# Performance work log

Hardware: AMD Instinct MI355X
Metric: run time of the kernel (lower is better)

The kernel has to match this reference:

```python
import jax, jax.numpy as jnp
import numpy as np

D_MODEL = 1024
D_STATE = 16
D_CONV = 4
D_INNER = 2048  # expand * d_model
DT_RANK = 64    # ceil(d_model / 16)
EPS = 1e-6


def setup_inputs() -> dict:
    key = jax.random.key(0)
    ks = jax.random.split(key, 8)
    B, T = 2, 2048
    x = jax.random.normal(ks[0], (B, T, D_MODEL), dtype=jnp.float32)
    in_proj_w = jax.random.normal(ks[1], (2 * D_INNER, D_MODEL), dtype=jnp.float32) * (D_MODEL ** -0.5)
    conv_w = jax.random.normal(ks[2], (D_INNER, 1, D_CONV), dtype=jnp.float32) * 0.3
    conv_b = jnp.zeros((D_INNER,), dtype=jnp.float32)
    x_proj_w = jax.random.normal(ks[3], (DT_RANK + 2 * D_STATE, D_INNER), dtype=jnp.float32) * (D_INNER ** -0.5)
    dt_std = DT_RANK ** -0.5
    dt_proj_w = jax.random.uniform(ks[4], (D_INNER, DT_RANK), minval=-dt_std, maxval=dt_std, dtype=jnp.float32)
    dt = jnp.exp(jax.random.uniform(ks[5], (D_INNER,), dtype=jnp.float32) * (np.log(0.1) - np.log(0.001)) + np.log(0.001))
    dt_proj_b = dt + jnp.log(-jnp.expm1(-dt))
    A_log = jnp.log(jnp.tile(jnp.arange(1, D_STATE + 1, dtype=jnp.float32)[None, :], (D_INNER, 1)))
    D = jnp.ones((D_INNER,), dtype=jnp.float32)
    out_proj_w = jax.random.normal(ks[6], (D_MODEL, D_INNER), dtype=jnp.float32) * (D_INNER ** -0.5)
    norm_w = jnp.ones((D_MODEL,), dtype=jnp.float32)
    return dict(x=x, in_proj_w=in_proj_w, conv_w=conv_w, conv_b=conv_b,
                x_proj_w=x_proj_w, dt_proj_w=dt_proj_w, dt_proj_b=dt_proj_b,
                A_log=A_log, D=D, out_proj_w=out_proj_w, norm_w=norm_w)


def _mamba_fwd(x, in_proj_w, conv_w, conv_b, x_proj_w, dt_proj_w, dt_proj_b,
               A_log, D, out_proj_w, norm_w):
    residual = x
    # RMSNorm (no mean subtraction)
    xn = x / jnp.sqrt(jnp.mean(x * x, axis=-1, keepdims=True) + EPS) * norm_w
    # in_proj -> [B,T,2*d_inner]
    xz = xn @ in_proj_w.T
    x_s, z = xz[..., :D_INNER], xz[..., D_INNER:]
    # depthwise causal conv1d (left pad d_conv-1, keep first T outputs)
    xc = jax.lax.conv_general_dilated(
        x_s.transpose(0, 2, 1), conv_w, window_strides=(1,),
        padding=[(D_CONV - 1, 0)], dimension_numbers=('NCH', 'OIH', 'NCH'),
        feature_group_count=D_INNER)
    x_conv = jax.nn.silu(xc + conv_b[None, :, None]).transpose(0, 2, 1)  # [B,T,d_inner]
    # x_proj -> (dt_raw, B_ssm, C_ssm)
    x_dbc = x_conv @ x_proj_w.T
    dt_raw = x_dbc[..., :DT_RANK]
    B_ssm = x_dbc[..., DT_RANK:DT_RANK + D_STATE]   # [B,T,d_state]
    C_ssm = x_dbc[..., DT_RANK + D_STATE:]          # [B,T,d_state]
    delta = jax.nn.softplus(dt_raw @ dt_proj_w.T + dt_proj_b)  # [B,T,d_inner]
    A = -jnp.exp(A_log)  # [d_inner, d_state]
    # selective scan (ZOH discretisation) with clamped delta
    dc = jnp.clip(delta, -10.0, 1.0)
    du = dc * x_conv
    Bsz = x.shape[0]
    h0 = jnp.zeros((Bsz, D_INNER, D_STATE), dtype=x.dtype)

    def step(h, inp):
        d_t, du_t, b_t, c_t = inp  # [B,di],[B,di],[B,ds],[B,ds]
        dA = jnp.exp(d_t[:, :, None] * A[None])            # [B,di,ds]
        h = dA * h + du_t[:, :, None] * b_t[:, None, :]
        y = jnp.einsum('bis,bs->bi', h, c_t)
        return h, y

    xs = (dc.transpose(1, 0, 2), du.transpose(1, 0, 2),
          B_ssm.transpose(1, 0, 2), C_ssm.transpose(1, 0, 2))
    _, ys = jax.lax.scan(step, h0, xs)           # ys: [T,B,d_inner]
    y = ys.transpose(1, 0, 2) + x_conv * D       # + skip D term
    y = y * jax.nn.silu(z)                       # gate
    return y @ out_proj_w.T + residual


def reference(x, in_proj_w, conv_w, conv_b, x_proj_w, dt_proj_w, dt_proj_b,
              A_log, D, out_proj_w, norm_w):
    return _mamba_fwd(x, in_proj_w, conv_w, conv_b, x_proj_w, dt_proj_w,
                      dt_proj_b, A_log, D, out_proj_w, norm_w)
```

## Files before the change

kernel.cpp:

```cpp
#include <hip/hip_runtime.h>
#include <hip/hip_bf16.h>

typedef float f32x4 __attribute__((ext_vector_type(4)));
typedef __bf16 bf16x8 __attribute__((ext_vector_type(8)));
typedef unsigned short us8 __attribute__((ext_vector_type(8)));
typedef _Float16 f16x8 __attribute__((ext_vector_type(8)));

#define D_MODEL 1024
#define D_INNER 2048
#define D_STATE 16
#define DT_RANK 64
#define NTOK 4096
#define TSEQ 2048
#define NS32 64

__device__ __forceinline__ unsigned short f2bf(float f) {
  unsigned int u = __builtin_bit_cast(unsigned int, f);
  u += 0x7fffu + ((u >> 16) & 1u);
  return (unsigned short)(u >> 16);
}
__device__ __forceinline__ float bf2f(unsigned short u) {
  return __builtin_bit_cast(float, (unsigned int)u << 16);
}

__device__ __forceinline__ void gload_lds16(const unsigned short* g,
                                            unsigned short* l) {
  __builtin_amdgcn_global_load_lds(
      (const __attribute__((address_space(1))) void*)g,
      (__attribute__((address_space(3))) void*)l, 16, 0, 0);
}

__global__ __launch_bounds__(256) void k_prep(
    const float* __restrict__ x, const float* __restrict__ nw,
    unsigned short* __restrict__ xn,
    const float* __restrict__ w_in, const float* __restrict__ w_xp,
    const float* __restrict__ w_dt, const float* __restrict__ w_out,
    unsigned short* __restrict__ o_in, unsigned short* __restrict__ o_xp,
    unsigned short* __restrict__ o_dt, unsigned short* __restrict__ o_out) {
  int bid = blockIdx.x;
  int tid = threadIdx.x;
  if (bid < 4096) {
    const float4 v = *(const float4*)&x[(size_t)bid * 1024 + tid * 4];
    const float4 w = *(const float4*)&nw[tid * 4];
    float ss = v.x * v.x + v.y * v.y + v.z * v.z + v.w * v.w;
#pragma unroll
    for (int o = 32; o >= 1; o >>= 1) ss += __shfl_xor(ss, o);
    __shared__ float red[4];
    if ((tid & 63) == 0) red[tid >> 6] = ss;
    __syncthreads();
    ss = red[0] + red[1] + red[2] + red[3];
    float rs = rsqrtf(ss * (1.0f / 1024.0f) + 1e-6f);
    ushort4 o4;
    o4.x = f2bf(v.x * rs * w.x);
    o4.y = f2bf(v.y * rs * w.y);
    o4.z = f2bf(v.z * rs * w.z);
    o4.w = f2bf(v.w * rs * w.w);
    *(ushort4*)&xn[(size_t)bid * 1024 + tid * 4] = o4;
    return;
  }
  int idx = (bid - 4096) * 256 + tid;
  const float* src;
  unsigned short* dst;
  int rel;
  if (idx < 1048576) { src = w_in; dst = o_in; rel = idx; }
  else if (idx < 1097728) { src = w_xp; dst = o_xp; rel = idx - 1048576; }
  else if (idx < 1114112) {
    ushort4 z = {0, 0, 0, 0};
    *(ushort4*)&o_xp[196608 + (size_t)(idx - 1097728) * 4] = z;
    return;
  }
  else if (idx < 1146880) { src = w_dt; dst = o_dt; rel = idx - 1114112; }
  else { src = w_out; dst = o_out; rel = idx - 1146880; }
  float4 v = ((const float4*)src)[rel];
  ushort4 o;
  o.x = f2bf(v.x); o.y = f2bf(v.y); o.z = f2bf(v.z); o.w = f2bf(v.w);
  ((ushort4*)dst)[rel] = o;
}

template <int BM, int BN, int WAVES_M, int WAVES_N, int EPI, int KSPLIT>
__device__ __forceinline__ void gemm_body(
    const unsigned short* __restrict__ A, const unsigned short* __restrict__ Bw,
    void* __restrict__ Cout, int M, int N, int K,
    const float* __restrict__ epi) {
  constexpr int BK = 64;
  constexpr int TM = BM / (WAVES_M * 16);
  constexpr int TN = BN / (WAVES_N * 16);
  __shared__ __align__(16) unsigned short As[BM * BK];
  __shared__ __align__(16) unsigned short Bs[BN * BK];
  const int tid = threadIdx.x;
  const int wave = tid >> 6, lane = tid & 63;
  const int wm = wave / WAVES_N, wn = wave % WAVES_N;
  const int m0 = blockIdx.x * BM, n0 = blockIdx.y * BN;
  const int lm = lane & 15, q = lane >> 4;
  const int lrow = lane >> 3;
  const int scol = ((lane & 7) ^ lrow) * 8;

  f32x4 acc[TM][TN] = {};

  const int k0 = (KSPLIT > 0) ? blockIdx.z * KSPLIT : 0;
  const int kend = (KSPLIT > 0) ? k0 + KSPLIT : K;

  for (int kb = k0; kb < kend; kb += BK) {
#pragma unroll
    for (int ii = 0; ii < BM / 32; ++ii) {
      int j = ii * 4 + wave;
      gload_lds16(&A[(size_t)(m0 + j * 8 + lrow) * K + kb + scol],
                  &As[j * 512 + lane * 8]);
    }
#pragma unroll
    for (int ii = 0; ii < BN / 32; ++ii) {
      int j = ii * 4 + wave;
      gload_lds16(&Bw[(size_t)(n0 + j * 8 + lrow) * K + kb + scol],
                  &Bs[j * 512 + lane * 8]);
    }
    __syncthreads();
#pragma unroll
    for (int ks = 0; ks < 2; ++ks) {
      const int pos = ((ks * 4 + q) ^ (lane & 7)) * 8;
      bf16x8 af[TM], bfr[TN];
#pragma unroll
      for (int tm = 0; tm < TM; ++tm)
        af[tm] = __builtin_bit_cast(
            bf16x8, *(const us8*)&As[(wm * TM * 16 + tm * 16 + lm) * BK + pos]);
#pragma unroll
      for (int tn = 0; tn < TN; ++tn)
        bfr[tn] = __builtin_bit_cast(
            bf16x8, *(const us8*)&Bs[(wn * TN * 16 + tn * 16 + lm) * BK + pos]);
#pragma unroll
      for (int tm = 0; tm < TM; ++tm)
#pragma unroll
        for (int tn = 0; tn < TN; ++tn)
          acc[tm][tn] = __builtin_amdgcn_mfma_f32_16x16x32_bf16(
              af[tm], bfr[tn], acc[tm][tn], 0, 0, 0);
    }
    __syncthreads();
  }

#pragma unroll
  for (int tm = 0; tm < TM; ++tm)
#pragma unroll
    for (int tn = 0; tn < TN; ++tn)
#pragma unroll
      for (int r = 0; r < 4; ++r) {
        int mg = m0 + wm * TM * 16 + tm * 16 + q * 4 + r;
        int ng = n0 + wn * TN * 16 + tn * 16 + lm;
        float v = acc[tm][tn][r];
        if (EPI == 0) {
          ((_Float16*)Cout)[(size_t)mg * N + ng] = (_Float16)v;
        } else if (EPI == 2) {
          ((float*)Cout)[(size_t)mg * N + ng] = v + epi[(size_t)mg * N + ng];
        } else if (EPI == 5) {
          if (ng < 96)
            ((float*)Cout)[((size_t)blockIdx.z * NTOK + mg) * 96 + ng] = v;
        }
      }
}

__global__ __launch_bounds__(256) void g_inproj(
    const unsigned short* __restrict__ A, const unsigned short* __restrict__ B,
    void* __restrict__ C) {
  gemm_body<128, 128, 2, 2, 0, 0>(A, B, C, NTOK, 4096, 1024, nullptr);
}
__global__ __launch_bounds__(256) void g_outproj(
    const unsigned short* __restrict__ A, const unsigned short* __restrict__ B,
    void* __restrict__ C, const float* __restrict__ epi) {
  gemm_body<64, 128, 2, 2, 2, 0>(A, B, C, NTOK, 1024, 2048, epi);
}

__global__ __launch_bounds__(256) void g_xprojconv(
    const _Float16* __restrict__ xz, const float* __restrict__ cw,
    const float* __restrict__ cbp, const unsigned short* __restrict__ Bw,
    float* __restrict__ Cout, unsigned short* __restrict__ xcb) {
  constexpr int K = 2048;
  __shared__ __align__(16) unsigned short As[64 * 64];
  __shared__ __align__(16) unsigned short Bs[128 * 64];
  const int tid = threadIdx.x;
  const int wave = tid >> 6, lane = tid & 63;
  const int wm = wave >> 1, wn = wave & 1;
  const int m0 = blockIdx.x * 64, n0 = 0;
  const int lm = lane & 15, q = lane >> 4;
  const int lrow = lane >> 3;
  const int scol = ((lane & 7) ^ lrow) * 8;

  f32x4 acc[2][4] = {};
  const int k0 = blockIdx.z * 256;

  for (int kb = k0; kb < k0 + 256; kb += 64) {
#pragma unroll
    for (int ii = 0; ii < 2; ++ii) {
      int j = ii * 4 + wave;
      int r = j * 8 + lrow;
      int m = m0 + r;
      int t = m & (TSEQ - 1);
      int c = kb + scol;
      float4 cb0 = *(const float4*)&cbp[c];
      float4 cb1 = *(const float4*)&cbp[c + 4];
      float a[8] = {cb0.x, cb0.y, cb0.z, cb0.w, cb1.x, cb1.y, cb1.z, cb1.w};
      float w8[8][4];
#pragma unroll
      for (int e = 0; e < 8; ++e) {
        float4 wv = *(const float4*)&cw[(c + e) * 4];
        w8[e][0] = wv.x; w8[e][1] = wv.y; w8[e][2] = wv.z; w8[e][3] = wv.w;
      }
#pragma unroll
      for (int jj = 0; jj < 4; ++jj) {
        bool ok = (t - 3 + jj) >= 0;
        int msrc = ok ? (m - 3 + jj) : m;
        float g = ok ? 1.0f : 0.0f;
        f16x8 xv = *(const f16x8*)&xz[(size_t)msrc * 4096 + c];
#pragma unroll
        for (int e = 0; e < 8; ++e) a[e] += g * w8[e][jj] * (float)xv[e];
      }
      us8 ov;
#pragma unroll
      for (int e = 0; e < 8; ++e) {
        float sg = 1.0f / (1.0f + __expf(-a[e]));
        ov[e] = f2bf(a[e] * sg);
      }
      *(us8*)&As[j * 512 + lane * 8] = ov;
      *(us8*)&xcb[(size_t)m * 2048 + c] = ov;
    }
#pragma unroll
    for (int ii = 0; ii < 4; ++ii) {
      int j = ii * 4 + wave;
      gload_lds16(&Bw[(size_t)(n0 + j * 8 + lrow) * K + kb + scol],
                  &Bs[j * 512 + lane * 8]);
    }
    __syncthreads();
#pragma unroll
    for (int ks = 0; ks < 2; ++ks) {
      const int pos = ((ks * 4 + q) ^ (lane & 7)) * 8;
      bf16x8 af[2], bfr[4];
#pragma unroll
      for (int tm = 0; tm < 2; ++tm)
        af[tm] = __builtin_bit_cast(
            bf16x8, *(const us8*)&As[(wm * 32 + tm * 16 + lm) * 64 + pos]);
#pragma unroll
      for (int tn = 0; tn < 4; ++tn)
        bfr[tn] = __builtin_bit_cast(
            bf16x8, *(const us8*)&Bs[(wn * 64 + tn * 16 + lm) * 64 + pos]);
#pragma unroll
      for (int tm = 0; tm < 2; ++tm)
#pragma unroll
        for (int tn = 0; tn < 4; ++tn)
          acc[tm][tn] = __builtin_amdgcn_mfma_f32_16x16x32_bf16(
              af[tm], bfr[tn], acc[tm][tn], 0, 0, 0);
    }
    __syncthreads();
  }

#pragma unroll
  for (int tm = 0; tm < 2; ++tm)
#pragma unroll
    for (int tn = 0; tn < 4; ++tn)
#pragma unroll
      for (int r = 0; r < 4; ++r) {
        int mg = m0 + wm * 32 + tm * 16 + q * 4 + r;
        int ng = n0 + wn * 64 + tn * 16 + lm;
        if (ng < 96)
          Cout[((size_t)blockIdx.z * NTOK + mg) * 96 + ng] = acc[tm][tn][r];
      }
}

__global__ __launch_bounds__(256) void k_xreduce(
    const float* __restrict__ part, float* __restrict__ xdbc,
    unsigned short* __restrict__ dtb) {
  int quad = blockIdx.x * 256 + threadIdx.x;
  float4 s = ((const float4*)part)[quad];
#pragma unroll
  for (int z = 1; z < 8; ++z) {
    float4 p = ((const float4*)part)[(size_t)z * 98304 + quad];
    s.x += p.x; s.y += p.y; s.z += p.z; s.w += p.w;
  }
  ((float4*)xdbc)[quad] = s;
  int col4 = (quad % 24) * 4;
  if (col4 < 64) {
    int m = quad / 24;
    ushort4 o;
    o.x = f2bf(s.x); o.y = f2bf(s.y); o.z = f2bf(s.z); o.w = f2bf(s.w);
    *(ushort4*)&dtb[(size_t)m * 64 + col4] = o;
  }
}

__global__ __launch_bounds__(256, 4) void k_dtscan(
    const unsigned short* __restrict__ dtb, const unsigned short* __restrict__ wdt,
    const float* __restrict__ dt_b, const unsigned short* __restrict__ xcb,
    const float* __restrict__ xdbc, _Float16* __restrict__ dcb,
    float* __restrict__ hend32, float* __restrict__ sdc32) {
  __shared__ __align__(16) unsigned short lds[18688];
  _Float16* dcs = (_Float16*)lds;
  float* sB = (float*)&lds[8448];
  unsigned short* xcs = &lds[10496];
  const int tid = threadIdx.x;
  const int wave = tid >> 6, lane = tid & 63;
  const int wm = wave >> 1, wn = wave & 1;
  const int m0 = blockIdx.x * 64, n0 = blockIdx.y * 128;
  const int lm = lane & 15, q = lane >> 4;

#pragma unroll
  for (int i = 0; i < 4; ++i) {
    int flat = i * 256 + tid;
    int t = flat >> 4, c8 = (flat & 15) * 8;
    gload_lds16(&xcb[(size_t)(m0 + t) * 2048 + n0 + c8],
                &xcs[(size_t)flat * 8]);
  }
  {
    int t = tid >> 2, c4 = (tid & 3) * 4;
    gload_lds16((const unsigned short*)&xdbc[(size_t)(m0 + t) * 96 + 64 + c4],
                (unsigned short*)&sB[tid * 4]);
  }

  float bias_v[4];
#pragma unroll
  for (int tn = 0; tn < 4; ++tn) bias_v[tn] = dt_b[n0 + wn * 64 + tn * 16 + lm];

  f32x4 acc[2][4] = {};
  const unsigned short* Ab = &dtb[(size_t)(m0 + wm * 32 + lm) * 64];
  const unsigned short* Bb = &wdt[(size_t)(n0 + wn * 64 + lm) * 64];
#pragma unroll
  for (int ks = 0; ks < 2; ++ks) {
    const int pos = ks * 32 + q * 8;
    bf16x8 af[2], bfr[4];
#pragma unroll
    for (int tm = 0; tm < 2; ++tm)
      af[tm] = __builtin_bit_cast(bf16x8, *(const us8*)&Ab[tm * 1024 + pos]);
#pragma unroll
    for (int tn = 0; tn < 4; ++tn)
      bfr[tn] = __builtin_bit_cast(bf16x8, *(const us8*)&Bb[tn * 1024 + pos]);
#pragma unroll
    for (int tm = 0; tm < 2; ++tm)
#pragma unroll
      for (int tn = 0; tn < 4; ++tn)
        acc[tm][tn] = __builtin_amdgcn_mfma_f32_16x16x32_bf16(
            af[tm], bfr[tn], acc[tm][tn], 0, 0, 0);
  }

  float dck[2][4][4];
#pragma unroll
  for (int tm = 0; tm < 2; ++tm)
#pragma unroll
    for (int tn = 0; tn < 4; ++tn)
#pragma unroll
      for (int r = 0; r < 4; ++r) {
        int mgl = wm * 32 + tm * 16 + q * 4 + r;
        int ngl = wn * 64 + tn * 16 + lm;
        float rr = acc[tm][tn][r] + bias_v[tn];
        float dc = fminf(__logf(1.0f + __expf(rr)), 1.0f);
        dck[tm][tn][r] = dc;
        dcs[mgl * 132 + ngl] = (_Float16)dc;
      }
  __syncthreads();

#pragma unroll
  for (int tm = 0; tm < 2; ++tm)
#pragma unroll
    for (int tn = 0; tn < 4; ++tn)
#pragma unroll
      for (int r = 0; r < 4; ++r) {
        int mgl = wm * 32 + tm * 16 + q * 4 + r;
        int ngl = wn * 64 + tn * 16 + lm;
        dcb[(size_t)(m0 + mgl) * 2048 + n0 + ngl] = (_Float16)dck[tm][tn][r];
      }

  int ch2 = tid & 127, sg = tid >> 7;
  int gch = n0 + ch2;
  int gt0 = m0 + sg * 32;
  int b = gt0 >> 11, s32 = (gt0 & 2047) >> 5;
  size_t base = ((size_t)(b * NS32 + s32) * 2048 + gch);
  float h[16];
#pragma unroll
  for (int s = 0; s < 16; ++s) h[s] = 0.f;
  float Sdc = 0.f;
#pragma unroll 4
  for (int tt = 0; tt < 32; ++tt) {
    int t = sg * 32 + tt;
    float dcv = (float)dcs[t * 132 + ch2];
    float xc = bf2f(xcs[t * 128 + ch2]);
    float qq = __expf(-dcv);
    float du = dcv * xc;
    Sdc += dcv;
    float qp[16];
    qp[0] = qq;
#pragma unroll
    for (int i = 1; i < 16; ++i) qp[i] = qp[i >> 1] * qp[i - (i >> 1) - 1];
    float4 b0 = *(const float4*)&sB[t * 16 + 0];
    float4 b1 = *(const float4*)&sB[t * 16 + 4];
    float4 b2 = *(const float4*)&sB[t * 16 + 8];
    float4 b3 = *(const float4*)&sB[t * 16 + 12];
    float Bv[16] = {b0.x, b0.y, b0.z, b0.w, b1.x, b1.y, b1.z, b1.w,
                    b2.x, b2.y, b2.z, b2.w, b3.x, b3.y, b3.z, b3.w};
#pragma unroll
    for (int s = 0; s < 16; ++s) h[s] = qp[s] * h[s] + du * Bv[s];
  }
#pragma unroll
  for (int s4 = 0; s4 < 4; ++s4)
    *(float4*)&hend32[base * 16 + s4 * 4] = make_float4(
        h[s4 * 4], h[s4 * 4 + 1], h[s4 * 4 + 2], h[s4 * 4 + 3]);
  sdc32[base] = Sdc;
}

__global__ __launch_bounds__(256) void k_scan2(
    const float* __restrict__ hend32, const float* __restrict__ sdc32,
    float* __restrict__ hin32) {
  int idx = blockIdx.x * 256 + threadIdx.x;
  int s = idx & 15, ch = (idx >> 4) & 2047, b = idx >> 15;
  float sp1 = (float)(s + 1);
  float H = 0.f;
  for (int j0 = 0; j0 < NS32; j0 += 8) {
    float he[8], S[8];
#pragma unroll
    for (int k = 0; k < 8; ++k) {
      size_t base = ((size_t)(b * NS32 + j0 + k) * 2048 + ch);
      he[k] = hend32[base * 16 + s];
      S[k] = sdc32[base];
    }
#pragma unroll
    for (int k = 0; k < 8; ++k) {
      size_t base = ((size_t)(b * NS32 + j0 + k) * 2048 + ch);
      hin32[base * 16 + s] = H;
      H = __expf(-S[k] * sp1) * H + he[k];
    }
  }
}

__global__ __launch_bounds__(256) void k_scan3(
    const _Float16* __restrict__ dc, const unsigned short* __restrict__ xcb,
    const float* __restrict__ xdbc, const _Float16* __restrict__ xz,
    const float* __restrict__ hin32, const float* __restrict__ Dp,
    unsigned short* __restrict__ ybf) {
  int bid = blockIdx.x;
  int chg = bid & 7, seg = (bid >> 3) & 63, b = bid >> 9;
  int tid = threadIdx.x;
  int ch = chg * 256 + tid;
  int mbase = b * TSEQ + seg * 32;
  int ch0 = chg * 256;

  __shared__ __align__(16) unsigned short l3[26624];
  _Float16* sdc = (_Float16*)l3;
  unsigned short* sxc = l3 + 8192;
  _Float16* sz = (_Float16*)(l3 + 16384);
  float* sBC = (float*)(l3 + 24576);

#pragma unroll
  for (int i = 0; i < 4; ++i) {
    int flat = i * 256 + tid;
    int tt = flat >> 5, c8 = (flat & 31) * 8;
    gload_lds16((const unsigned short*)&dc[(size_t)(mbase + tt) * 2048 + ch0 + c8],
                (unsigned short*)&sdc[(size_t)flat * 8]);
  }
#pragma unroll
  for (int i = 0; i < 4; ++i) {
    int flat = i * 256 + tid;
    int tt = flat >> 5, c8 = (flat & 31) * 8;
    gload_lds16(&xcb[(size_t)(mbase + tt) * 2048 + ch0 + c8],
                &sxc[(size_t)flat * 8]);
  }
#pragma unroll
  for (int i = 0; i < 4; ++i) {
    int flat = i * 256 + tid;
    int tt = flat >> 5, c8 = (flat & 31) * 8;
    gload_lds16((const unsigned short*)&xz[(size_t)(mbase + tt) * 4096 + 2048 + ch0 + c8],
                (unsigned short*)&sz[(size_t)flat * 8]);
  }
  {
    int t = tid >> 3, c4 = (tid & 7) * 4;
    gload_lds16((const unsigned short*)&xdbc[(size_t)(mbase + t) * 96 + 64 + c4],
                (unsigned short*)&sBC[t * 32 + c4]);
  }

  size_t base = ((size_t)(b * NS32 + seg) * 2048 + ch);
  float h[16];
#pragma unroll
  for (int s4 = 0; s4 < 4; ++s4) {
    float4 hv = *(const float4*)&hin32[base * 16 + s4 * 4];
    h[s4 * 4] = hv.x; h[s4 * 4 + 1] = hv.y;
    h[s4 * 4 + 2] = hv.z; h[s4 * 4 + 3] = hv.w;
  }
  float Dv = Dp[ch];
  __syncthreads();

#pragma unroll 2
  for (int tt = 0; tt < 32; ++tt) {
    float dcv = (float)sdc[tt * 256 + tid];
    float xc = bf2f(sxc[tt * 256 + tid]);
    float z = (float)sz[tt * 256 + tid];
    float qv = __expf(-dcv);
    float du = dcv * xc;
    float qp[16];
    qp[0] = qv;
#pragma unroll
    for (int i = 1; i < 16; ++i) qp[i] = qp[i >> 1] * qp[i - (i >> 1) - 1];
    float4 b0 = *(const float4*)&sBC[tt * 32 + 0];
    float4 b1 = *(const float4*)&sBC[tt * 32 + 4];
    float4 b2 = *(const float4*)&sBC[tt * 32 + 8];
    float4 b3 = *(const float4*)&sBC[tt * 32 + 12];
    float4 c0 = *(const float4*)&sBC[tt * 32 + 16];
    float4 c1 = *(const float4*)&sBC[tt * 32 + 20];
    float4 c2 = *(const float4*)&sBC[tt * 32 + 24];
    float4 c3 = *(const float4*)&sBC[tt * 32 + 28];
    float Bv[16] = {b0.x, b0.y, b0.z, b0.w, b1.x, b1.y, b1.z, b1.w,
                    b2.x, b2.y, b2.z, b2.w, b3.x, b3.y, b3.z, b3.w};
    float Cv[16] = {c0.x, c0.y, c0.z, c0.w, c1.x, c1.y, c1.z, c1.w,
                    c2.x, c2.y, c2.z, c2.w, c3.x, c3.y, c3.z, c3.w};
    float y = 0.f;
#pragma unroll
    for (int s = 0; s < 16; ++s) {
      h[s] = qp[s] * h[s] + du * Bv[s];
      y += h[s] * Cv[s];
    }
    float yv = y + xc * Dv;
    float yf = yv * z / (1.0f + __expf(-z));
    ybf[(size_t)(mbase + tt) * 2048 + ch] = f2bf(yf);
  }
}

extern "C" void kernel_launch(void* const* d_in, const int* in_sizes, int n_in,
                              void* d_out, int out_size, void* d_ws, size_t ws_size,
                              hipStream_t stream) {
  (void)in_sizes; (void)n_in; (void)out_size; (void)ws_size;
  const float* x      = (const float*)d_in[0];
  const float* w_in   = (const float*)d_in[1];
  const float* conv_w = (const float*)d_in[2];
  const float* conv_b = (const float*)d_in[3];
  const float* w_xp   = (const float*)d_in[4];
  const float* w_dt   = (const float*)d_in[5];
  const float* dt_b   = (const float*)d_in[6];
  const float* Dp     = (const float*)d_in[8];
  const float* w_out  = (const float*)d_in[9];
  const float* nw     = (const float*)d_in[10];
  float* out = (float*)d_out;

  char* ws = (char*)d_ws;
  size_t off = 0;
  auto carve = [&](size_t bytes) {
    char* p = ws + off;
    off = (off + bytes + 255) & ~(size_t)255;
    return p;
  };
  unsigned short* xn_bf   = (unsigned short*)carve(8388608);
  unsigned short* w_in_bf = (unsigned short*)carve(8388608);
  unsigned short* w_xp_bf = (unsigned short*)carve(524288);
  unsigned short* w_dt_bf = (unsigned short*)carve(262144);
  unsigned short* w_out_bf= (unsigned short*)carve(4194304);
  _Float16* xz            = (_Float16*)carve(33554432);
  unsigned short* xcb     = (unsigned short*)carve(16777216);
  float* xdbc             = (float*)carve(1572864);
  unsigned short* dtb     = (unsigned short*)carve(524288);
  _Float16* dcb           = (_Float16*)carve(16777216);
  unsigned short* ybf     = (unsigned short*)carve(16777216);
  float* sdc32            = (float*)carve(1048576);
  float* hin32            = (float*)carve(16777216);
  float* xpart            = (float*)carve(12582912);
  float* hend32 = (float*)xn_bf;

  k_prep<<<10624, 256, 0, stream>>>(x, nw, xn_bf, w_in, w_xp, w_dt, w_out,
                                    w_in_bf, w_xp_bf, w_dt_bf, w_out_bf);

  g_inproj<<<dim3(32, 32), 256, 0, stream>>>(xn_bf, w_in_bf, xz);

  g_xprojconv<<<dim3(64, 1, 8), 256, 0, stream>>>(xz, conv_w, conv_b,
                                                  w_xp_bf, xpart, xcb);
  k_xreduce<<<384, 256, 0, stream>>>(xpart, xdbc, dtb);

  k_dtscan<<<dim3(64, 16), 256, 0, stream>>>(dtb, w_dt_bf, dt_b, xcb, xdbc,
                                             dcb, hend32, sdc32);

  k_scan2<<<256, 256, 0, stream>>>(hend32, sdc32, hin32);
  k_scan3<<<1024, 256, 0, stream>>>(dcb, xcb, xdbc, xz, hin32, Dp, ybf);

  g_outproj<<<dim3(64, 8), 256, 0, stream>>>(ybf, w_out_bf, out, x);
}
```

Before: 271.7 us.

## Recompute delta in scan3 instead of storing dcb from dtscan

Drops the fp16 delta buffer that k_dtscan wrote and k_scan3 read back. k_scan3 now recomputes delta for its 32-token by 256-channel tile with a small MFMA over dt_rank, then applies the softplus and clamp. It also streams z from global memory through a 4-deep register prefetch instead of staging it in LDS, which shrinks shared memory and adds an occupancy hint. The cost is that the small dt projection GEMM is now computed twice, and z is read with strided per-thread global loads.

```diff
diff --git a/kernel.cpp b/kernel.cpp
--- a/kernel.cpp
+++ b/kernel.cpp
@@ -285,7 +285,7 @@
 __global__ __launch_bounds__(256, 4) void k_dtscan(
     const unsigned short* __restrict__ dtb, const unsigned short* __restrict__ wdt,
     const float* __restrict__ dt_b, const unsigned short* __restrict__ xcb,
-    const float* __restrict__ xdbc, _Float16* __restrict__ dcb,
+    const float* __restrict__ xdbc,
     float* __restrict__ hend32, float* __restrict__ sdc32) {
   __shared__ __align__(16) unsigned short lds[18688];
   _Float16* dcs = (_Float16*)lds;
@@ -335,7 +335,6 @@
             af[tm], bfr[tn], acc[tm][tn], 0, 0, 0);
   }
 
-  float dck[2][4][4];
 #pragma unroll
   for (int tm = 0; tm < 2; ++tm)
 #pragma unroll
@@ -346,21 +345,9 @@
         int ngl = wn * 64 + tn * 16 + lm;
         float rr = acc[tm][tn][r] + bias_v[tn];
         float dc = fminf(__logf(1.0f + __expf(rr)), 1.0f);
-        dck[tm][tn][r] = dc;
         dcs[mgl * 132 + ngl] = (_Float16)dc;
       }
   __syncthreads();
-
-#pragma unroll
-  for (int tm = 0; tm < 2; ++tm)
-#pragma unroll
-    for (int tn = 0; tn < 4; ++tn)
-#pragma unroll
-      for (int r = 0; r < 4; ++r) {
-        int mgl = wm * 32 + tm * 16 + q * 4 + r;
-        int ngl = wn * 64 + tn * 16 + lm;
-        dcb[(size_t)(m0 + mgl) * 2048 + n0 + ngl] = (_Float16)dck[tm][tn][r];
-      }
 
   int ch2 = tid & 127, sg = tid >> 7;
   int gch = n0 + ch2;
@@ -423,8 +410,9 @@
   }
 }
 
-__global__ __launch_bounds__(256) void k_scan3(
-    const _Float16* __restrict__ dc, const unsigned short* __restrict__ xcb,
+__global__ __launch_bounds__(256, 4) void k_scan3(
+    const unsigned short* __restrict__ dtb, const unsigned short* __restrict__ wdt,
+    const float* __restrict__ dt_b, const unsigned short* __restrict__ xcb,
     const float* __restrict__ xdbc, const _Float16* __restrict__ xz,
     const float* __restrict__ hin32, const float* __restrict__ Dp,
     unsigned short* __restrict__ ybf) {
@@ -435,19 +423,11 @@
   int mbase = b * TSEQ + seg * 32;
   int ch0 = chg * 256;
 
-  __shared__ __align__(16) unsigned short l3[26624];
+  __shared__ __align__(16) unsigned short l3[18432];
   _Float16* sdc = (_Float16*)l3;
   unsigned short* sxc = l3 + 8192;
-  _Float16* sz = (_Float16*)(l3 + 16384);
-  float* sBC = (float*)(l3 + 24576);
-
-#pragma unroll
-  for (int i = 0; i < 4; ++i) {
-    int flat = i * 256 + tid;
-    int tt = flat >> 5, c8 = (flat & 31) * 8;
-    gload_lds16((const unsigned short*)&dc[(size_t)(mbase + tt) * 2048 + ch0 + c8],
-                (unsigned short*)&sdc[(size_t)flat * 8]);
-  }
+  float* sBC = (float*)(l3 + 16384);
+
 #pragma unroll
   for (int i = 0; i < 4; ++i) {
     int flat = i * 256 + tid;
@@ -455,19 +435,51 @@
     gload_lds16(&xcb[(size_t)(mbase + tt) * 2048 + ch0 + c8],
                 &sxc[(size_t)flat * 8]);
   }
-#pragma unroll
-  for (int i = 0; i < 4; ++i) {
-    int flat = i * 256 + tid;
-    int tt = flat >> 5, c8 = (flat & 31) * 8;
-    gload_lds16((const unsigned short*)&xz[(size_t)(mbase + tt) * 4096 + 2048 + ch0 + c8],
-                (unsigned short*)&sz[(size_t)flat * 8]);
-  }
   {
     int t = tid >> 3, c4 = (tid & 7) * 4;
     gload_lds16((const unsigned short*)&xdbc[(size_t)(mbase + t) * 96 + 64 + c4],
                 (unsigned short*)&sBC[t * 32 + c4]);
   }
 
+  const int wave = tid >> 6, lane = tid & 63;
+  const int lm = lane & 15, q = lane >> 4;
+  float bias_v[4];
+#pragma unroll
+  for (int tn = 0; tn < 4; ++tn)
+    bias_v[tn] = dt_b[ch0 + wave * 64 + tn * 16 + lm];
+  f32x4 acc[2][4] = {};
+  const unsigned short* Ab = &dtb[(size_t)(mbase + lm) * 64];
+  const unsigned short* Bb = &wdt[(size_t)(ch0 + wave * 64 + lm) * 64];
+#pragma unroll
+  for (int ks = 0; ks < 2; ++ks) {
+    const int pos = ks * 32 + q * 8;
+    bf16x8 af[2], bfr[4];
+#pragma unroll
+    for (int tm = 0; tm < 2; ++tm)
+      af[tm] = __builtin_bit_cast(bf16x8, *(const us8*)&Ab[tm * 1024 + pos]);
+#pragma unroll
+    for (int tn = 0; tn < 4; ++tn)
+      bfr[tn] = __builtin_bit_cast(bf16x8, *(const us8*)&Bb[tn * 1024 + pos]);
+#pragma unroll
+    for (int tm = 0; tm < 2; ++tm)
+#pragma unroll
+      for (int tn = 0; tn < 4; ++tn)
+        acc[tm][tn] = __builtin_amdgcn_mfma_f32_16x16x32_bf16(
+            af[tm], bfr[tn], acc[tm][tn], 0, 0, 0);
+  }
+#pragma unroll
+  for (int tm = 0; tm < 2; ++tm)
+#pragma unroll
+    for (int tn = 0; tn < 4; ++tn)
+#pragma unroll
+      for (int r = 0; r < 4; ++r) {
+        int t = tm * 16 + q * 4 + r;
+        int c = wave * 64 + tn * 16 + lm;
+        float rr = acc[tm][tn][r] + bias_v[tn];
+        float dc = fminf(__logf(1.0f + __expf(rr)), 1.0f);
+        sdc[t * 256 + c] = (_Float16)dc;
+      }
+
   size_t base = ((size_t)(b * NS32 + seg) * 2048 + ch);
   float h[16];
 #pragma unroll
@@ -477,13 +489,19 @@
     h[s4 * 4 + 2] = hv.z; h[s4 * 4 + 3] = hv.w;
   }
   float Dv = Dp[ch];
+  float zbuf[4];
+#pragma unroll
+  for (int p = 0; p < 4; ++p)
+    zbuf[p] = (float)xz[(size_t)(mbase + p) * 4096 + 2048 + ch];
   __syncthreads();
 
-#pragma unroll 2
+#pragma unroll 4
   for (int tt = 0; tt < 32; ++tt) {
     float dcv = (float)sdc[tt * 256 + tid];
     float xc = bf2f(sxc[tt * 256 + tid]);
-    float z = (float)sz[tt * 256 + tid];
+    float z = zbuf[tt & 3];
+    int tpf = (tt + 4 < 32) ? tt + 4 : 31;
+    zbuf[tt & 3] = (float)xz[(size_t)(mbase + tpf) * 4096 + 2048 + ch];
     float qv = __expf(-dcv);
     float du = dcv * xc;
     float qp[16];
@@ -546,7 +564,6 @@
   unsigned short* xcb     = (unsigned short*)carve(16777216);
   float* xdbc             = (float*)carve(1572864);
   unsigned short* dtb     = (unsigned short*)carve(524288);
-  _Float16* dcb           = (_Float16*)carve(16777216);
   unsigned short* ybf     = (unsigned short*)carve(16777216);
   float* sdc32            = (float*)carve(1048576);
   float* hin32            = (float*)carve(16777216);
@@ -563,10 +580,11 @@
   k_xreduce<<<384, 256, 0, stream>>>(xpart, xdbc, dtb);
 
   k_dtscan<<<dim3(64, 16), 256, 0, stream>>>(dtb, w_dt_bf, dt_b, xcb, xdbc,
-                                             dcb, hend32, sdc32);
+                                             hend32, sdc32);
 
   k_scan2<<<256, 256, 0, stream>>>(hend32, sdc32, hin32);
-  k_scan3<<<1024, 256, 0, stream>>>(dcb, xcb, xdbc, xz, hin32, Dp, ybf);
+  k_scan3<<<1024, 256, 0, stream>>>(dtb, w_dt_bf, dt_b, xcb, xdbc, xz,
+                                    hin32, Dp, ybf);
 
   g_outproj<<<dim3(64, 8), 256, 0, stream>>>(ybf, w_out_bf, out, x);
 }
```

Result: slower. 283.9 us (+4.5%).
